# Performance work log

Hardware: AMD Instinct MI355X
Metric: run time of the kernel (lower is better)

## Reference

```python
import jax, jax.numpy as jnp
import numpy as np

EPS = 1e-5

def layer_norm(x, w, b):
    mu = x.mean(-1, keepdims=True)
    var = x.var(-1, keepdims=True)
    return (x - mu) / jnp.sqrt(var + EPS) * w + b

def s5_forward(u, Lambda_re, Lambda_im, B_re, B_im, C_re, C_im, D, log_step):
    # u: [B, L, H]; diagonal S5 SSM with P complex states, ZOH discretization.
    Lam = (Lambda_re + 1j * Lambda_im).astype(jnp.complex64)          # [P]
    dt = jnp.exp(log_step).astype(jnp.complex64)                       # [P]
    Lam_bar = jnp.exp(Lam * dt)                                        # [P]
    Bc = (B_re + 1j * B_im).astype(jnp.complex64)                      # [P, H]
    B_bar = ((Lam_bar - 1.0) / Lam)[:, None] * Bc                      # [P, H]
    Bu = jnp.einsum('blh,ph->blp', u.astype(jnp.complex64), B_bar)     # [B, L, P]
    A = jnp.broadcast_to(Lam_bar, Bu.shape)                            # [B, L, P]

    def binop(e1, e2):
        a1, b1 = e1
        a2, b2 = e2
        return (a2 * a1, a2 * b1 + b2)

    _, xs = jax.lax.associative_scan(binop, (A, Bu), axis=1)           # [B, L, P]
    Cc = (C_re + 1j * C_im).astype(jnp.complex64)                      # [H, P]
    y = 2.0 * jnp.einsum('blp,hp->blh', xs, Cc).real + D * u           # [B, L, H]
    return y

def setup_inputs() -> dict:
    key = jax.random.key(0)
    ks = jax.random.split(key, 12)
    B, L, H, P = 4, 4096, 512, 512
    x = jax.random.normal(ks[0], (B, L, H), jnp.float32)
    # SSM params (HiPPO-like flavor: negative real part, spread imaginary part)
    Lambda_re = -(0.5 * jax.random.uniform(ks[1], (P,), jnp.float32) + 0.1)
    Lambda_im = jnp.pi * jnp.arange(P, dtype=jnp.float32)
    B_re = jax.random.normal(ks[2], (P, H), jnp.float32) / np.sqrt(2.0 * H)
    B_im = jax.random.normal(ks[3], (P, H), jnp.float32) / np.sqrt(2.0 * H)
    C_re = jax.random.normal(ks[4], (H, P), jnp.float32) / np.sqrt(P)
    C_im = jax.random.normal(ks[5], (H, P), jnp.float32) / np.sqrt(P)
    D = jax.random.normal(ks[6], (H,), jnp.float32)
    log_step = jax.random.uniform(ks[7], (P,), jnp.float32,
                                  minval=np.log(1e-3), maxval=np.log(1e-1))
    ln1_w = jnp.ones((H,), jnp.float32); ln1_b = jnp.zeros((H,), jnp.float32)
    ln2_w = jnp.ones((H,), jnp.float32); ln2_b = jnp.zeros((H,), jnp.float32)
    W_enc = jax.random.normal(ks[8], (2 * H, H), jnp.float32) / np.sqrt(H)
    W_dec = jax.random.normal(ks[9], (H, H), jnp.float32) / np.sqrt(H)
    return {"x": x, "ln1_w": ln1_w, "ln1_b": ln1_b,
            "Lambda_re": Lambda_re, "Lambda_im": Lambda_im,
            "B_re": B_re, "B_im": B_im, "C_re": C_re, "C_im": C_im,
            "D": D, "log_step": log_step,
            "ln2_w": ln2_w, "ln2_b": ln2_b, "W_enc": W_enc, "W_dec": W_dec}

def reference(x, ln1_w, ln1_b, Lambda_re, Lambda_im, B_re, B_im, C_re, C_im,
              D, log_step, ln2_w, ln2_b, W_enc, W_dec):
    fx = layer_norm(x, ln1_w, ln1_b)
    res = fx
    u = s5_forward(fx, Lambda_re, Lambda_im, B_re, B_im, C_re, C_im, D, log_step)
    h = jax.nn.gelu(u, approximate=False) + res  # eval mode: dropout = identity
    fx2 = layer_norm(h, ln2_w, ln2_b)
    e = fx2 @ W_enc.T                              # [B, L, 2H]
    a, g = jnp.split(e, 2, axis=-1)
    ff = a * jax.nn.gelu(g, approximate=False)     # GEGLU
    out = ff @ W_dec.T + fx2
    return out
```

## Files before the change

### kernel.cpp

```cpp
#include <hip/hip_runtime.h>
#include <math.h>

#define Bz 4
#define Lz 4096
#define Hz 512
#define Pz 512
#define Nz (Bz*Lz)
#define CL 64
#define NC (Lz/CL)
#define CS (Bz*NC*Pz)
#define EPSf 1e-5f

typedef unsigned short u16;
typedef unsigned int   u32;
typedef __attribute__((ext_vector_type(8))) short bf16x8;
typedef __attribute__((ext_vector_type(4))) float f32x4;

__device__ __forceinline__ float gelu_exact(float x){
    return 0.5f * x * (1.0f + erff(x * 0.70710678118654752f));
}
__device__ __forceinline__ u16 f2b(float f){
    union { float f; u32 u; } v; v.f = f;
    u32 u = v.u;
    u32 r = (u + 0x7FFFu + ((u >> 16) & 1u)) >> 16;
    return (u16)r;
}
__device__ __forceinline__ float b2f(u16 h){
    union { u32 u; float f; } v; v.u = ((u32)h) << 16; return v.f;
}
__device__ __forceinline__ float cvt_in(float x){ return x; }
__device__ __forceinline__ float cvt_in(u16 x){ return b2f(x); }

__device__ __forceinline__ void gload_lds16(const u16* g, u16* l){
    __builtin_amdgcn_global_load_lds(
        (const __attribute__((address_space(1))) void*)g,
        (__attribute__((address_space(3))) void*)l, 16, 0, 0);
}

__global__ void setup_kernel(const float* __restrict__ Lre, const float* __restrict__ Lim,
                             const float* __restrict__ log_step,
                             float* __restrict__ prm){
    int p = blockIdx.x*blockDim.x + threadIdx.x;
    if (p >= Pz) return;
    float lr = Lre[p], li = Lim[p];
    float dt = expf(log_step[p]);
    float ar = lr*dt, ai = li*dt;
    float e = expf(ar);
    float Abr = e*cosf(ai), Abi = e*sinf(ai);
    prm[p]        = Abr;
    prm[Pz + p]   = Abi;
    float nr = Abr - 1.0f, ni = Abi;
    float d2 = lr*lr + li*li;
    prm[2*Pz + p] = (nr*lr + ni*li)/d2;
    prm[3*Pz + p] = (ni*lr - nr*li)/d2;
    float arC = ar*(float)CL, aiC = ai*(float)CL;
    float eC = expf(arC);
    prm[4*Pz + p] = eC*cosf(aiC);
    prm[5*Pz + p] = eC*sinf(aiC);
}

__global__ __launch_bounds__(256) void cvt_all(const float* __restrict__ B_re,
                                               const float* __restrict__ B_im,
                                               const float* __restrict__ C_re,
                                               const float* __restrict__ C_im,
                                               const float* __restrict__ W_enc,
                                               const float* __restrict__ W_dec,
                                               u16* __restrict__ Bcat,
                                               u16* __restrict__ Ccat,
                                               u16* __restrict__ Wenc,
                                               u16* __restrict__ Wdec){
    const int Q = 512*512;
    int i = blockIdx.x*256 + threadIdx.x;
    if (i < Q){ Bcat[i] = f2b(B_re[i]); return; }
    i -= Q;
    if (i < Q){ Bcat[Q + i] = f2b(B_im[i]); return; }
    i -= Q;
    if (i < Q){
        int h = i >> 9, p = i & 511;
        Ccat[(size_t)h*1024 + p]       = f2b(C_re[i]);
        Ccat[(size_t)h*1024 + 512 + p] = f2b(-C_im[i]);
        return;
    }
    i -= Q;
    if (i < 2*Q){ Wenc[i] = f2b(W_enc[i]); return; }
    i -= 2*Q;
    Wdec[i] = f2b(W_dec[i]);
}

template<typename T>
__global__ __launch_bounds__(256) void ln_kernel(const T* __restrict__ in,
                                                 const float* __restrict__ w,
                                                 const float* __restrict__ b,
                                                 u16* __restrict__ ob){
    int row = blockIdx.x;
    int tid = threadIdx.x;
    const T* r = in + (size_t)row*Hz;
    float v0 = cvt_in(r[tid]), v1 = cvt_in(r[tid+256]);
    float s = v0+v1, q = v0*v0+v1*v1;
    #pragma unroll
    for (int o=32;o;o>>=1){ s += __shfl_down(s,o); q += __shfl_down(q,o); }
    __shared__ float ss[4], sq[4];
    __shared__ float mu_s, rs_s;
    int wid = tid>>6, lane = tid&63;
    if (lane==0){ ss[wid]=s; sq[wid]=q; }
    __syncthreads();
    if (tid==0){
        float S=ss[0]+ss[1]+ss[2]+ss[3];
        float Q=sq[0]+sq[1]+sq[2]+sq[3];
        float mu = S/(float)Hz;
        float var = Q/(float)Hz - mu*mu;
        mu_s = mu; rs_s = rsqrtf(var + EPSf);
    }
    __syncthreads();
    float mu = mu_s, rs = rs_s;
    u16* o = ob + (size_t)row*Hz;
    o[tid]     = f2b((v0-mu)*rs*w[tid]    +b[tid]);
    o[tid+256] = f2b((v1-mu)*rs*w[tid+256]+b[tid+256]);
}

#define EB16 0
#define EY   1
#define ERES 2

__device__ __forceinline__ void stage64(const u16* __restrict__ src, int ld,
                                        int grow0, int kt, u16* ldsQ){
    int lane = threadIdx.x & 63;
    int w    = threadIdx.x >> 6;
    int r    = w*8 + (lane >> 3);
    int colE = 8*((lane & 7) ^ ((lane >> 3) & 7));
    const u16* g = src + (size_t)(grow0 + r)*ld + kt + colE;
    gload_lds16(g, ldsQ + w*512);
}

template<int K, int BN, int EPI>
__global__ __launch_bounds__(512, 2)
void gemm2p(const u16* __restrict__ A, const u16* __restrict__ Bw, int M,
            u16* __restrict__ outB,
            const u16* __restrict__ fxB,
            const float* __restrict__ Dv,
            const u16* __restrict__ resB,
            float* __restrict__ outF)
{
    constexpr int NT = K/64;
    constexpr int WR = (BN==256)?16:8;
    __shared__ u16 AL[2][256*64];
    __shared__ u16 BL[2][BN*64];

    int nx = gridDim.x, ny = gridDim.y;
    int nwg = nx*ny;
    int lid = blockIdx.x + blockIdx.y*nx;
    int cpx = nwg >> 3;
    int gdx = (lid & 7)*cpx + (lid >> 3);
    int n0 = (gdx / ny) * 256;
    int m0 = (gdx % ny) * BN;

    int l = threadIdx.x & 63;
    int w = threadIdx.x >> 6;
    int lrow  = l & 15;
    int lcol0 = ((l >> 4)*8) ^ ((l & 7) << 3);
    int lcol1 = lcol0 ^ 32;
    int row0w = (BN==256)? 0 : (w>>2)*128;
    int colw  = (BN==256)? w*32 : (w&3)*32;

    f32x4 acc[WR][2];
    #pragma unroll
    for (int i=0;i<WR;++i){ acc[i][0]=(f32x4)(0.f); acc[i][1]=(f32x4)(0.f); }

    #pragma unroll
    for (int q=0;q<4;++q) stage64(A, K, n0+q*64, 0, &AL[0][q*4096]);
    #pragma unroll
    for (int q=0;q<BN/64;++q) stage64(Bw, K, m0+q*64, 0, &BL[0][q*4096]);
    __syncthreads();

    for (int T=0; T<NT; ++T){
        int buf = T & 1, nb = buf ^ 1;
        if (T+1 < NT){
            int ktn = (T+1)*64;
            #pragma unroll
            for (int q=0;q<4;++q) stage64(A, K, n0+q*64, ktn, &AL[nb][q*4096]);
            #pragma unroll
            for (int q=0;q<BN/64;++q) stage64(Bw, K, m0+q*64, ktn, &BL[nb][q*4096]);
        }
        const u16* Ab = &AL[buf][0];
        const u16* Bb = &BL[buf][0];
        bf16x8 bfr[2][2];
        #pragma unroll
        for (int fn=0; fn<2; ++fn){
            bfr[0][fn] = *(const bf16x8*)&Bb[(colw + fn*16 + lrow)*64 + lcol0];
            bfr[1][fn] = *(const bf16x8*)&Bb[(colw + fn*16 + lrow)*64 + lcol1];
        }
        #pragma unroll
        for (int mh=0; mh<WR/8; ++mh){
            #pragma unroll
            for (int ks=0; ks<2; ++ks){
                bf16x8 af[8];
                #pragma unroll
                for (int f=0;f<8;++f)
                    af[f] = *(const bf16x8*)&Ab[(row0w + mh*128 + f*16 + lrow)*64 + (ks? lcol1 : lcol0)];
                #pragma unroll
                for (int f=0;f<8;++f)
                    #pragma unroll
                    for (int fn=0;fn<2;++fn)
                        acc[mh*8+f][fn] = __builtin_amdgcn_mfma_f32_16x16x32_bf16(af[f], bfr[ks][fn], acc[mh*8+f][fn], 0,0,0);
            }
        }
        __syncthreads();
    }

    int er = (l >> 4) * 4;
    int ec = l & 15;
    #pragma unroll
    for (int fm=0; fm<WR; ++fm)
        #pragma unroll
        for (int fn=0; fn<2; ++fn)
            #pragma unroll
            for (int q=0; q<4; ++q){
                int n = n0 + row0w + fm*16 + er + q;
                int m = m0 + colw + fn*16 + ec;
                float v = acc[fm][fn][q];
                if (EPI == EB16){
                    outB[(size_t)n*M + m] = f2b(v);
                } else if (EPI == EY){
                    size_t idx = (size_t)n*Hz + m;
                    float fxv = b2f(fxB[idx]);
                    float y = 2.0f*v + Dv[m]*fxv;
                    outB[idx] = f2b(gelu_exact(y) + fxv);
                } else {
                    size_t idx = (size_t)n*Hz + m;
                    outF[idx] = v + b2f(resB[idx]);
                }
            }
}

__global__ __launch_bounds__(256) void scan_phase1(const u16* __restrict__ g,
                                                   const float* __restrict__ prm,
                                                   float* __restrict__ ERe,
                                                   float* __restrict__ EIm){
    int t = blockIdx.x;
    int pb = t & 1; t >>= 1;
    int c  = t % NC; t /= NC;
    int b  = t;
    int p  = pb*256 + threadIdx.x;
    size_t base = ((size_t)(b*Lz + c*CL))*1024 + p;
    float Ar = prm[p], Ai = prm[Pz+p];
    float fre = prm[2*Pz+p], fim = prm[3*Pz+p];
    float xr = 0.f, xi = 0.f;
    for (int ll = 0; ll < CL; ++ll) {
        float gr = b2f(g[base]), gi = b2f(g[base+512]);
        float br = fre*gr - fim*gi;
        float bi = fre*gi + fim*gr;
        float nr = Ar*xr - Ai*xi + br;
        float ni = Ar*xi + Ai*xr + bi;
        xr = nr; xi = ni;
        base += 1024;
    }
    size_t ci = ((size_t)(b*NC + c))*Pz + p;
    ERe[ci] = xr; EIm[ci] = xi;
}

__global__ __launch_bounds__(256) void scan_combine(const float* __restrict__ ERe,
                                                    const float* __restrict__ EIm,
                                                    const float* __restrict__ prm,
                                                    float* __restrict__ SinRe,
                                                    float* __restrict__ SinIm){
    int gt = blockIdx.x*256 + threadIdx.x;
    int b = gt / Pz, p = gt % Pz;
    float Ar = prm[4*Pz+p], Ai = prm[5*Pz+p];
    float Sr = 0.f, Si = 0.f;
    for (int c = 0; c < NC; ++c) {
        size_t idx = ((size_t)(b*NC + c))*Pz + p;
        SinRe[idx] = Sr; SinIm[idx] = Si;
        float er = ERe[idx], ei = EIm[idx];
        float nr = Ar*Sr - Ai*Si + er;
        float ni = Ar*Si + Ai*Sr + ei;
        Sr = nr; Si = ni;
    }
}

__global__ __launch_bounds__(256) void scan_phase2(u16* __restrict__ g,
                                                   const float* __restrict__ prm,
                                                   const float* __restrict__ SinRe,
                                                   const float* __restrict__ SinIm){
    int t = blockIdx.x;
    int pb = t & 1; t >>= 1;
    int c  = t % NC; t /= NC;
    int b  = t;
    int p  = pb*256 + threadIdx.x;
    size_t base = ((size_t)(b*Lz + c*CL))*1024 + p;
    size_t ci = ((size_t)(b*NC + c))*Pz + p;
    float Ar = prm[p], Ai = prm[Pz+p];
    float fre = prm[2*Pz+p], fim = prm[3*Pz+p];
    float xr = SinRe[ci], xi = SinIm[ci];
    for (int ll = 0; ll < CL; ++ll) {
        float gr = b2f(g[base]), gi = b2f(g[base+512]);
        float br = fre*gr - fim*gi;
        float bi = fre*gi + fim*gr;
        float nr = Ar*xr - Ai*xi + br;
        float ni = Ar*xi + Ai*xr + bi;
        xr = nr; xi = ni;
        g[base] = f2b(xr); g[base+512] = f2b(xi);
        base += 1024;
    }
}

__global__ __launch_bounds__(256) void geglu_kernel(const u16* __restrict__ e,
                                                    u16* __restrict__ ff){
    size_t i = (size_t)blockIdx.x*256 + threadIdx.x;
    int n = (int)(i >> 9), m = (int)(i & 511);
    float a = b2f(e[(size_t)n*1024 + m]);
    float gg = b2f(e[(size_t)n*1024 + 512 + m]);
    ff[i] = f2b(a * gelu_exact(gg));
}

extern "C" void kernel_launch(void* const* d_in, const int* in_sizes, int n_in,
                              void* d_out, int out_size, void* d_ws, size_t ws_size,
                              hipStream_t stream) {
    const float* x        = (const float*)d_in[0];
    const float* ln1_w    = (const float*)d_in[1];
    const float* ln1_b    = (const float*)d_in[2];
    const float* Lre      = (const float*)d_in[3];
    const float* Lim      = (const float*)d_in[4];
    const float* B_re     = (const float*)d_in[5];
    const float* B_im     = (const float*)d_in[6];
    const float* C_re     = (const float*)d_in[7];
    const float* C_im     = (const float*)d_in[8];
    const float* Dv       = (const float*)d_in[9];
    const float* log_step = (const float*)d_in[10];
    const float* ln2_w    = (const float*)d_in[11];
    const float* ln2_b    = (const float*)d_in[12];
    const float* W_enc    = (const float*)d_in[13];
    const float* W_dec    = (const float*)d_in[14];
    float* out = (float*)d_out;

    const size_t NH = (size_t)Nz*Hz;
    char* W = (char*)d_ws;
    u16*   fxb  = (u16*)  (W);
    u16*   g    = (u16*)  (W + NH*2);
    u16*   hb   = (u16*)  (W + NH*6);
    u16*   fx2b = (u16*)  (W + NH*8);
    float* ERe  = (float*)(W + NH*10);
    float* EIm  = ERe + CS;
    float* SinRe= EIm + CS;
    float* SinIm= SinRe + CS;
    float* prm  = SinIm + CS;
    u16*   Bcat = (u16*)(prm + 6*Pz);
    u16*   Ccat = Bcat + 1024*512;
    u16*   Wenc = Ccat + 512*1024;
    u16*   Wdec = Wenc + 1024*512;

    setup_kernel<<<dim3(2), dim3(256), 0, stream>>>(Lre, Lim, log_step, prm);

    cvt_all<<<dim3(6*1024), dim3(256), 0, stream>>>(B_re, B_im, C_re, C_im, W_enc, W_dec,
                                                    Bcat, Ccat, Wenc, Wdec);

    ln_kernel<float><<<dim3(Nz), dim3(256), 0, stream>>>(x, ln1_w, ln1_b, fxb);

    gemm2p<512,256,EB16><<<dim3(Nz/256, 1024/256), dim3(512), 0, stream>>>(
        fxb, Bcat, 1024, g, nullptr, nullptr, nullptr, nullptr);

    scan_phase1<<<dim3(Bz*NC*2), dim3(256), 0, stream>>>(g, prm, ERe, EIm);
    scan_combine<<<dim3((Bz*Pz)/256), dim3(256), 0, stream>>>(ERe, EIm, prm, SinRe, SinIm);
    scan_phase2<<<dim3(Bz*NC*2), dim3(256), 0, stream>>>(g, prm, SinRe, SinIm);

    gemm2p<1024,128,EY><<<dim3(Nz/256, 512/128), dim3(512), 0, stream>>>(
        g, Ccat, 512, hb, fxb, Dv, nullptr, nullptr);

    ln_kernel<u16><<<dim3(Nz), dim3(256), 0, stream>>>(hb, ln2_w, ln2_b, fx2b);

    gemm2p<512,256,EB16><<<dim3(Nz/256, 1024/256), dim3(512), 0, stream>>>(
        fx2b, Wenc, 1024, g, nullptr, nullptr, nullptr, nullptr);

    geglu_kernel<<<dim3((unsigned)(NH/256)), dim3(256), 0, stream>>>(g, fxb);

    gemm2p<512,128,ERES><<<dim3(Nz/256, 512/128), dim3(512), 0, stream>>>(
        fxb, Wdec, 512, nullptr, nullptr, nullptr, fx2b, out);
}
```

Baseline: 195.8 us.

## Replace tiled GEMMs with full-row GEMMs fusing LayerNorm and GEGLU MLP

Swaps the generic 256-row tiled GEMM for 64-row blocks that each compute a full output row width of 512. This lets the second LayerNorm run inside the C-projection epilogue and the whole GEGLU MLP (encode, gate, decode) run in one kernel with the intermediate held in LDS. It removes the LN2 and GEGLU launches and the global round trips for the h, e and ff tensors. The cost is smaller M tiles with a K step of 32, which means more barriers, lower MFMA reuse per block, and a large LDS footprint in the fused MLP that may limit occupancy.

```diff
diff --git a/kernel.cpp b/kernel.cpp
--- a/kernel.cpp
+++ b/kernel.cpp
@@ -87,15 +87,14 @@
     Wdec[i] = f2b(W_dec[i]);
 }
 
-template<typename T>
-__global__ __launch_bounds__(256) void ln_kernel(const T* __restrict__ in,
+__global__ __launch_bounds__(256) void ln_kernel(const float* __restrict__ in,
                                                  const float* __restrict__ w,
                                                  const float* __restrict__ b,
                                                  u16* __restrict__ ob){
     int row = blockIdx.x;
     int tid = threadIdx.x;
-    const T* r = in + (size_t)row*Hz;
-    float v0 = cvt_in(r[tid]), v1 = cvt_in(r[tid+256]);
+    const float* r = in + (size_t)row*Hz;
+    float v0 = r[tid], v1 = r[tid+256];
     float s = v0+v1, q = v0*v0+v1*v1;
     #pragma unroll
     for (int o=32;o;o>>=1){ s += __shfl_down(s,o); q += __shfl_down(q,o); }
@@ -118,117 +117,301 @@
     o[tid+256] = f2b((v1-mu)*rs*w[tid+256]+b[tid+256]);
 }
 
-#define EB16 0
-#define EY   1
-#define ERES 2
-
-__device__ __forceinline__ void stage64(const u16* __restrict__ src, int ld,
-                                        int grow0, int kt, u16* ldsQ){
-    int lane = threadIdx.x & 63;
-    int w    = threadIdx.x >> 6;
-    int r    = w*8 + (lane >> 3);
-    int colE = 8*((lane & 7) ^ ((lane >> 3) & 7));
-    const u16* g = src + (size_t)(grow0 + r)*ld + kt + colE;
-    gload_lds16(g, ldsQ + w*512);
-}
-
-template<int K, int BN, int EPI>
+
+__device__ __forceinline__ void stageA64(const u16* __restrict__ src, int ld,
+                                         int row0, int kt, u16* lds){
+    int tid = threadIdx.x;
+    if (tid < 256){
+        int lane = tid & 63, c = tid >> 6;
+        int r = c*16 + (lane >> 2);
+        int colE = 8*((lane & 3) ^ ((lane >> 3) & 3));
+        gload_lds16(src + (size_t)(row0 + r)*ld + kt + colE, lds + c*512);
+    }
+}
+__device__ __forceinline__ void stageB512(const u16* __restrict__ src, int ld,
+                                          int row0, int kt, u16* lds){
+    int lane = threadIdx.x & 63, w = threadIdx.x >> 6;
+    #pragma unroll
+    for (int q = 0; q < 4; ++q){
+        int c = w + q*8;
+        int r = c*16 + (lane >> 2);
+        int colE = 8*((lane & 3) ^ ((lane >> 3) & 3));
+        gload_lds16(src + (size_t)(row0 + r)*ld + kt + colE, lds + c*512);
+    }
+}
+
 __global__ __launch_bounds__(512, 2)
-void gemm2p(const u16* __restrict__ A, const u16* __restrict__ Bw, int M,
-            u16* __restrict__ outB,
-            const u16* __restrict__ fxB,
-            const float* __restrict__ Dv,
-            const u16* __restrict__ resB,
-            float* __restrict__ outF)
-{
-    constexpr int NT = K/64;
-    constexpr int WR = (BN==256)?16:8;
-    __shared__ u16 AL[2][256*64];
-    __shared__ u16 BL[2][BN*64];
-
-    int nx = gridDim.x, ny = gridDim.y;
-    int nwg = nx*ny;
-    int lid = blockIdx.x + blockIdx.y*nx;
-    int cpx = nwg >> 3;
-    int gdx = (lid & 7)*cpx + (lid >> 3);
-    int n0 = (gdx / ny) * 256;
-    int m0 = (gdx % ny) * BN;
-
-    int l = threadIdx.x & 63;
-    int w = threadIdx.x >> 6;
-    int lrow  = l & 15;
-    int lcol0 = ((l >> 4)*8) ^ ((l & 7) << 3);
-    int lcol1 = lcol0 ^ 32;
-    int row0w = (BN==256)? 0 : (w>>2)*128;
-    int colw  = (BN==256)? w*32 : (w&3)*32;
-
-    f32x4 acc[WR][2];
-    #pragma unroll
-    for (int i=0;i<WR;++i){ acc[i][0]=(f32x4)(0.f); acc[i][1]=(f32x4)(0.f); }
-
-    #pragma unroll
-    for (int q=0;q<4;++q) stage64(A, K, n0+q*64, 0, &AL[0][q*4096]);
-    #pragma unroll
-    for (int q=0;q<BN/64;++q) stage64(Bw, K, m0+q*64, 0, &BL[0][q*4096]);
-    __syncthreads();
-
-    for (int T=0; T<NT; ++T){
+void gemm1_row(const u16* __restrict__ A, const u16* __restrict__ Bw,
+               u16* __restrict__ outB){
+    __shared__ u16 AL[2][64*32];
+    __shared__ u16 BL[2][512*32];
+    int lid = blockIdx.x;
+    int gdx = (lid & 7)*32 + (lid >> 3);
+    int n0 = gdx * 64;
+    int l = threadIdx.x & 63, w = threadIdx.x >> 6;
+    int lrow = l & 15;
+    int lcol = 8*((l >> 4) ^ ((l >> 1) & 3));
+    int er = (l >> 4)*4, ec = l & 15;
+
+    for (int ms = 0; ms < 2; ++ms){
+        f32x4 acc[4][4];
+        #pragma unroll
+        for (int i=0;i<4;++i)
+            #pragma unroll
+            for (int j=0;j<4;++j) acc[i][j] = (f32x4)(0.f);
+        stageA64(A, 512, n0, 0, &AL[0][0]);
+        stageB512(Bw, 512, ms*512, 0, &BL[0][0]);
+        __syncthreads();
+        for (int T=0; T<16; ++T){
+            int buf = T & 1, nb = buf ^ 1;
+            if (T+1 < 16){
+                stageA64(A, 512, n0, (T+1)*32, &AL[nb][0]);
+                stageB512(Bw, 512, ms*512, (T+1)*32, &BL[nb][0]);
+            }
+            bf16x8 bf4[4];
+            #pragma unroll
+            for (int fn=0; fn<4; ++fn)
+                bf4[fn] = *(const bf16x8*)&BL[buf][(w*64 + fn*16 + lrow)*32 + lcol];
+            #pragma unroll
+            for (int fm=0; fm<4; ++fm){
+                bf16x8 af = *(const bf16x8*)&AL[buf][(fm*16 + lrow)*32 + lcol];
+                #pragma unroll
+                for (int fn=0; fn<4; ++fn)
+                    acc[fm][fn] = __builtin_amdgcn_mfma_f32_16x16x32_bf16(af, bf4[fn], acc[fm][fn], 0,0,0);
+            }
+            __syncthreads();
+        }
+        #pragma unroll
+        for (int fm=0; fm<4; ++fm)
+            #pragma unroll
+            for (int fn=0; fn<4; ++fn)
+                #pragma unroll
+                for (int q=0; q<4; ++q){
+                    int n = n0 + fm*16 + er + q;
+                    int m = ms*512 + w*64 + fn*16 + ec;
+                    outB[(size_t)n*1024 + m] = f2b(acc[fm][fn][q]);
+                }
+    }
+}
+
+__global__ __launch_bounds__(512, 2)
+void gemm2_ln(const u16* __restrict__ A, const u16* __restrict__ Bw,
+              const u16* __restrict__ fxB, const float* __restrict__ Dv,
+              const float* __restrict__ w2, const float* __restrict__ b2,
+              u16* __restrict__ outB){
+    __shared__ u16 AL[2][64*32];
+    __shared__ u16 BL[2][512*32];
+    int lid = blockIdx.x;
+    int gdx = (lid & 7)*32 + (lid >> 3);
+    int n0 = gdx * 64;
+    int l = threadIdx.x & 63, w = threadIdx.x >> 6;
+    int lrow = l & 15;
+    int lcol = 8*((l >> 4) ^ ((l >> 1) & 3));
+    int er = (l >> 4)*4, ec = l & 15;
+
+    f32x4 acc[4][4];
+    #pragma unroll
+    for (int i=0;i<4;++i)
+        #pragma unroll
+        for (int j=0;j<4;++j) acc[i][j] = (f32x4)(0.f);
+    stageA64(A, 1024, n0, 0, &AL[0][0]);
+    stageB512(Bw, 1024, 0, 0, &BL[0][0]);
+    __syncthreads();
+    for (int T=0; T<32; ++T){
         int buf = T & 1, nb = buf ^ 1;
-        if (T+1 < NT){
-            int ktn = (T+1)*64;
-            #pragma unroll
-            for (int q=0;q<4;++q) stage64(A, K, n0+q*64, ktn, &AL[nb][q*4096]);
-            #pragma unroll
-            for (int q=0;q<BN/64;++q) stage64(Bw, K, m0+q*64, ktn, &BL[nb][q*4096]);
-        }
-        const u16* Ab = &AL[buf][0];
-        const u16* Bb = &BL[buf][0];
-        bf16x8 bfr[2][2];
-        #pragma unroll
-        for (int fn=0; fn<2; ++fn){
-            bfr[0][fn] = *(const bf16x8*)&Bb[(colw + fn*16 + lrow)*64 + lcol0];
-            bfr[1][fn] = *(const bf16x8*)&Bb[(colw + fn*16 + lrow)*64 + lcol1];
-        }
-        #pragma unroll
-        for (int mh=0; mh<WR/8; ++mh){
-            #pragma unroll
-            for (int ks=0; ks<2; ++ks){
-                bf16x8 af[8];
-                #pragma unroll
-                for (int f=0;f<8;++f)
-                    af[f] = *(const bf16x8*)&Ab[(row0w + mh*128 + f*16 + lrow)*64 + (ks? lcol1 : lcol0)];
-                #pragma unroll
-                for (int f=0;f<8;++f)
-                    #pragma unroll
-                    for (int fn=0;fn<2;++fn)
-                        acc[mh*8+f][fn] = __builtin_amdgcn_mfma_f32_16x16x32_bf16(af[f], bfr[ks][fn], acc[mh*8+f][fn], 0,0,0);
-            }
+        if (T+1 < 32){
+            stageA64(A, 1024, n0, (T+1)*32, &AL[nb][0]);
+            stageB512(Bw, 1024, 0, (T+1)*32, &BL[nb][0]);
+        }
+        bf16x8 bf4[4];
+        #pragma unroll
+        for (int fn=0; fn<4; ++fn)
+            bf4[fn] = *(const bf16x8*)&BL[buf][(w*64 + fn*16 + lrow)*32 + lcol];
+        #pragma unroll
+        for (int fm=0; fm<4; ++fm){
+            bf16x8 af = *(const bf16x8*)&AL[buf][(fm*16 + lrow)*32 + lcol];
+            #pragma unroll
+            for (int fn=0; fn<4; ++fn)
+                acc[fm][fn] = __builtin_amdgcn_mfma_f32_16x16x32_bf16(af, bf4[fn], acc[fm][fn], 0,0,0);
         }
         __syncthreads();
     }
 
-    int er = (l >> 4) * 4;
-    int ec = l & 15;
-    #pragma unroll
-    for (int fm=0; fm<WR; ++fm)
-        #pragma unroll
-        for (int fn=0; fn<2; ++fn)
+    float dvc[4], fxv;
+    #pragma unroll
+    for (int fn=0; fn<4; ++fn) dvc[fn] = Dv[w*64 + fn*16 + ec];
+    #pragma unroll
+    for (int fm=0; fm<4; ++fm)
+        #pragma unroll
+        for (int fn=0; fn<4; ++fn)
             #pragma unroll
             for (int q=0; q<4; ++q){
-                int n = n0 + row0w + fm*16 + er + q;
-                int m = m0 + colw + fn*16 + ec;
-                float v = acc[fm][fn][q];
-                if (EPI == EB16){
-                    outB[(size_t)n*M + m] = f2b(v);
-                } else if (EPI == EY){
-                    size_t idx = (size_t)n*Hz + m;
-                    float fxv = b2f(fxB[idx]);
-                    float y = 2.0f*v + Dv[m]*fxv;
-                    outB[idx] = f2b(gelu_exact(y) + fxv);
-                } else {
-                    size_t idx = (size_t)n*Hz + m;
-                    outF[idx] = v + b2f(resB[idx]);
-                }
+                int n = n0 + fm*16 + er + q;
+                int m = w*64 + fn*16 + ec;
+                fxv = b2f(fxB[(size_t)n*Hz + m]);
+                float y = 2.0f*acc[fm][fn][q] + dvc[fn]*fxv;
+                acc[fm][fn][q] = gelu_exact(y) + fxv;
+            }
+
+    float* S = (float*)&BL[0][0];
+    int tid = threadIdx.x;
+    if (tid < 128) S[tid] = 0.f;
+    __syncthreads();
+    #pragma unroll
+    for (int fm=0; fm<4; ++fm)
+        #pragma unroll
+        for (int q=0; q<4; ++q){
+            float sv = 0.f, qv = 0.f;
+            #pragma unroll
+            for (int fn=0; fn<4; ++fn){ float h = acc[fm][fn][q]; sv += h; qv += h*h; }
+            #pragma unroll
+            for (int o=1; o<16; o<<=1){ sv += __shfl_xor(sv, o); qv += __shfl_xor(qv, o); }
+            if (ec == 0){
+                int row = fm*16 + er + q;
+                atomicAdd(&S[row], sv);
+                atomicAdd(&S[64 + row], qv);
+            }
+        }
+    __syncthreads();
+    if (tid < 64){
+        float mu = S[tid] * (1.0f/512.0f);
+        float var = S[64 + tid] * (1.0f/512.0f) - mu*mu;
+        S[128 + tid] = mu;
+        S[192 + tid] = rsqrtf(var + EPSf);
+    }
+    __syncthreads();
+    float lw[4], lb[4];
+    #pragma unroll
+    for (int fn=0; fn<4; ++fn){ int m = w*64 + fn*16 + ec; lw[fn] = w2[m]; lb[fn] = b2[m]; }
+    #pragma unroll
+    for (int fm=0; fm<4; ++fm)
+        #pragma unroll
+        for (int q=0; q<4; ++q){
+            int row = fm*16 + er + q;
+            float mu = S[128 + row], rs = S[192 + row];
+            #pragma unroll
+            for (int fn=0; fn<4; ++fn){
+                int m = w*64 + fn*16 + ec;
+                float v = (acc[fm][fn][q] - mu)*rs*lw[fn] + lb[fn];
+                outB[(size_t)(n0 + row)*Hz + m] = f2b(v);
+            }
+        }
+}
+
+__global__ __launch_bounds__(512, 2)
+void mlp_fused(const u16* __restrict__ A , const u16* __restrict__ W1,
+               const u16* __restrict__ W2, float* __restrict__ outF){
+    __shared__ u16 AL[2][64*32];
+    __shared__ u16 BL[2][512*32];
+    __shared__ u16 FF[64*512];
+    int lid = blockIdx.x;
+    int gdx = (lid & 7)*32 + (lid >> 3);
+    int n0 = gdx * 64;
+    int l = threadIdx.x & 63, w = threadIdx.x >> 6;
+    int lrow = l & 15;
+    int lcol = 8*((l >> 4) ^ ((l >> 1) & 3));
+    int er = (l >> 4)*4, ec = l & 15;
+
+    f32x4 accA[4][4], accG[4][4];
+    #pragma unroll
+    for (int i=0;i<4;++i)
+        #pragma unroll
+        for (int j=0;j<4;++j){ accA[i][j]=(f32x4)(0.f); accG[i][j]=(f32x4)(0.f); }
+
+    stageA64(A, 512, n0, 0, &AL[0][0]);
+    stageB512(W1, 512, 0, 0, &BL[0][0]);
+    __syncthreads();
+    for (int T=0; T<16; ++T){
+        int buf = T & 1, nb = buf ^ 1;
+        if (T+1 < 16){
+            stageA64(A, 512, n0, (T+1)*32, &AL[nb][0]);
+            stageB512(W1, 512, 0, (T+1)*32, &BL[nb][0]);
+        }
+        bf16x8 bf4[4];
+        #pragma unroll
+        for (int fn=0; fn<4; ++fn)
+            bf4[fn] = *(const bf16x8*)&BL[buf][(w*64 + fn*16 + lrow)*32 + lcol];
+        #pragma unroll
+        for (int fm=0; fm<4; ++fm){
+            bf16x8 af = *(const bf16x8*)&AL[buf][(fm*16 + lrow)*32 + lcol];
+            #pragma unroll
+            for (int fn=0; fn<4; ++fn)
+                accA[fm][fn] = __builtin_amdgcn_mfma_f32_16x16x32_bf16(af, bf4[fn], accA[fm][fn], 0,0,0);
+        }
+        __syncthreads();
+    }
+    stageA64(A, 512, n0, 0, &AL[0][0]);
+    stageB512(W1, 512, 512, 0, &BL[0][0]);
+    __syncthreads();
+    for (int T=0; T<16; ++T){
+        int buf = T & 1, nb = buf ^ 1;
+        if (T+1 < 16){
+            stageA64(A, 512, n0, (T+1)*32, &AL[nb][0]);
+            stageB512(W1, 512, 512, (T+1)*32, &BL[nb][0]);
+        }
+        bf16x8 bf4[4];
+        #pragma unroll
+        for (int fn=0; fn<4; ++fn)
+            bf4[fn] = *(const bf16x8*)&BL[buf][(w*64 + fn*16 + lrow)*32 + lcol];
+        #pragma unroll
+        for (int fm=0; fm<4; ++fm){
+            bf16x8 af = *(const bf16x8*)&AL[buf][(fm*16 + lrow)*32 + lcol];
+            #pragma unroll
+            for (int fn=0; fn<4; ++fn)
+                accG[fm][fn] = __builtin_amdgcn_mfma_f32_16x16x32_bf16(af, bf4[fn], accG[fm][fn], 0,0,0);
+        }
+        __syncthreads();
+    }
+
+    #pragma unroll
+    for (int fm=0; fm<4; ++fm)
+        #pragma unroll
+        for (int fn=0; fn<4; ++fn)
+            #pragma unroll
+            for (int q=0; q<4; ++q){
+                int row = fm*16 + er + q;
+                int col = w*64 + fn*16 + ec;
+                float ffv = accA[fm][fn][q] * gelu_exact(accG[fm][fn][q]);
+                FF[row*512 + (((col >> 3) ^ (row & 7)) << 3) + (col & 7)] = f2b(ffv);
+            }
+    __syncthreads();
+
+    f32x4 accO[4][4];
+    #pragma unroll
+    for (int i=0;i<4;++i)
+        #pragma unroll
+        for (int j=0;j<4;++j) accO[i][j] = (f32x4)(0.f);
+    stageB512(W2, 512, 0, 0, &BL[0][0]);
+    __syncthreads();
+    for (int T=0; T<16; ++T){
+        int buf = T & 1, nb = buf ^ 1;
+        if (T+1 < 16)
+            stageB512(W2, 512, 0, (T+1)*32, &BL[nb][0]);
+        bf16x8 bf4[4];
+        #pragma unroll
+        for (int fn=0; fn<4; ++fn)
+            bf4[fn] = *(const bf16x8*)&BL[buf][(w*64 + fn*16 + lrow)*32 + lcol];
+        #pragma unroll
+        for (int fm=0; fm<4; ++fm){
+            int row = fm*16 + lrow;
+            int gr = (T*4 + (l >> 4)) ^ (l & 7);
+            bf16x8 af = *(const bf16x8*)&FF[row*512 + (gr << 3)];
+            #pragma unroll
+            for (int fn=0; fn<4; ++fn)
+                accO[fm][fn] = __builtin_amdgcn_mfma_f32_16x16x32_bf16(af, bf4[fn], accO[fm][fn], 0,0,0);
+        }
+        __syncthreads();
+    }
+
+    #pragma unroll
+    for (int fm=0; fm<4; ++fm)
+        #pragma unroll
+        for (int fn=0; fn<4; ++fn)
+            #pragma unroll
+            for (int q=0; q<4; ++q){
+                int n = n0 + fm*16 + er + q;
+                int m = w*64 + fn*16 + ec;
+                outF[(size_t)n*Hz + m] = accO[fm][fn][q] + b2f(A[(size_t)n*Hz + m]);
             }
 }
 
@@ -303,15 +486,6 @@
     }
 }
 
-__global__ __launch_bounds__(256) void geglu_kernel(const u16* __restrict__ e,
-                                                    u16* __restrict__ ff){
-    size_t i = (size_t)blockIdx.x*256 + threadIdx.x;
-    int n = (int)(i >> 9), m = (int)(i & 511);
-    float a = b2f(e[(size_t)n*1024 + m]);
-    float gg = b2f(e[(size_t)n*1024 + 512 + m]);
-    ff[i] = f2b(a * gelu_exact(gg));
-}
-
 extern "C" void kernel_launch(void* const* d_in, const int* in_sizes, int n_in,
                               void* d_out, int out_size, void* d_ws, size_t ws_size,
                               hipStream_t stream) {
@@ -336,9 +510,8 @@
     char* W = (char*)d_ws;
     u16*   fxb  = (u16*)  (W);
     u16*   g    = (u16*)  (W + NH*2);
-    u16*   hb   = (u16*)  (W + NH*6);
-    u16*   fx2b = (u16*)  (W + NH*8);
-    float* ERe  = (float*)(W + NH*10);
+    u16*   fx2b = (u16*)  (W + NH*6);
+    float* ERe  = (float*)(W + NH*8);
     float* EIm  = ERe + CS;
     float* SinRe= EIm + CS;
     float* SinIm= SinRe + CS;
@@ -353,25 +526,15 @@
     cvt_all<<<dim3(6*1024), dim3(256), 0, stream>>>(B_re, B_im, C_re, C_im, W_enc, W_dec,
                                                     Bcat, Ccat, Wenc, Wdec);
 
-    ln_kernel<float><<<dim3(Nz), dim3(256), 0, stream>>>(x, ln1_w, ln1_b, fxb);
-
-    gemm2p<512,256,EB16><<<dim3(Nz/256, 1024/256), dim3(512), 0, stream>>>(
-        fxb, Bcat, 1024, g, nullptr, nullptr, nullptr, nullptr);
+    ln_kernel<<<dim3(Nz), dim3(256), 0, stream>>>(x, ln1_w, ln1_b, fxb);
+
+    gemm1_row<<<dim3(Nz/64), dim3(512), 0, stream>>>(fxb, Bcat, g);
 
     scan_phase1<<<dim3(Bz*NC*2), dim3(256), 0, stream>>>(g, prm, ERe, EIm);
     scan_combine<<<dim3((Bz*Pz)/256), dim3(256), 0, stream>>>(ERe, EIm, prm, SinRe, SinIm);
     scan_phase2<<<dim3(Bz*NC*2), dim3(256), 0, stream>>>(g, prm, SinRe, SinIm);
 
-    gemm2p<1024,128,EY><<<dim3(Nz/256, 512/128), dim3(512), 0, stream>>>(
-        g, Ccat, 512, hb, fxb, Dv, nullptr, nullptr);
-
-    ln_kernel<u16><<<dim3(Nz), dim3(256), 0, stream>>>(hb, ln2_w, ln2_b, fx2b);
-
-    gemm2p<512,256,EB16><<<dim3(Nz/256, 1024/256), dim3(512), 0, stream>>>(
-        fx2b, Wenc, 1024, g, nullptr, nullptr, nullptr, nullptr);
-
-    geglu_kernel<<<dim3((unsigned)(NH/256)), dim3(256), 0, stream>>>(g, fxb);
-
-    gemm2p<512,128,ERES><<<dim3(Nz/256, 512/128), dim3(512), 0, stream>>>(
-        fxb, Wdec, 512, nullptr, nullptr, nullptr, fx2b, out);
-}
+    gemm2_ln<<<dim3(Nz/64), dim3(512), 0, stream>>>(g, Ccat, fxb, Dv, ln2_w, ln2_b, fx2b);
+
+    mlp_fused<<<dim3(Nz/64), dim3(512), 0, stream>>>(fx2b, Wenc, Wdec, out);
+}
```

Result: slower. 228.3 us (+16.6%).
